# Optimization experiments

Hardware: AMD Instinct MI355X
Metric: run time of the kernel (lower is better)

## Reference

```python
import jax, jax.numpy as jnp
import numpy as np

TAU = 2.0        # spikingjelly LIFNode default tau
VTH = 1.0        # v_threshold
ALPHA = 2.0      # ATan surrogate default alpha
NWIN = (4, 4, 4)
TOPK = 4
HEADS = 8

@jax.custom_vjp
def spike(x):
    return (x >= 0.0).astype(x.dtype)

def _spike_fwd(x):
    return spike(x), x

def _spike_bwd(x, g):
    # ATan surrogate: d/dx ~ alpha/2 / (1 + (pi/2 * alpha * x)^2)
    s = (jnp.pi / 2) * ALPHA * x
    return (g * (ALPHA / 2) / (1 + s * s),)

spike.defvjp(_spike_fwd, _spike_bwd)

def lif(x):
    # fresh-state single-step LIF: H = x/tau, spike if H >= v_threshold
    return spike(x / TAU - VTH)

def setup_inputs() -> dict:
    key = jax.random.key(0)
    ks = jax.random.split(key, 4)
    T, B, Lt, Lh, Lw, C = 4, 2, 8, 32, 32, 256
    x = jax.random.normal(ks[0], (T, B, Lt, Lh, Lw, C), jnp.float32)
    W_qkv = jax.random.normal(ks[1], (C, 3 * C), jnp.float32) / np.sqrt(C)
    b_qkv = jnp.zeros((3 * C,), jnp.float32)
    W_proj = jax.random.normal(ks[2], (C, C), jnp.float32) / np.sqrt(C)
    b_proj = jnp.zeros((C,), jnp.float32)
    return {"x": x, "W_qkv": W_qkv, "b_qkv": b_qkv, "W_proj": W_proj, "b_proj": b_proj}

def reference(x, W_qkv, b_qkv, W_proj, b_proj):
    T, B, Lt, Lh, Lw, C = x.shape
    wt, wh, ww = NWIN
    H = HEADS
    hd = C // H
    nw = wt * wh * ww
    pt, ph, pw = Lt // wt, Lh // wh, Lw // ww
    ws = pt * ph * pw

    # windowize: [T,B,nw,ws,C]
    xw = x.reshape(T, B, wt, pt, wh, ph, ww, pw, C)
    xw = xw.transpose(0, 1, 2, 4, 6, 3, 5, 7, 8).reshape(T, B, nw, ws, C)

    # region-level routing scores over windows
    region = xw.sum(0).mean(2)                                  # [B,nw,C]
    scores = jnp.einsum('bic,bjc->bij', region, region) * (hd ** -0.5)
    idx = jax.lax.top_k(scores, TOPK)[1]                        # [B,nw,topk]

    qkv = xw @ W_qkv + b_qkv                                    # [T,B,nw,ws,3C]
    q, k, v = jnp.split(qkv, 3, axis=-1)
    q, k, v = lif(q), lif(k), lif(v)
    q = q.reshape(T, B, nw, ws, H, hd)
    k = k.reshape(T, B, nw, ws, H, hd)
    v = v.reshape(T, B, nw, ws, H, hd)

    # per-batch gather of topk routed windows' k/v
    gather = jax.vmap(lambda kb, ib: kb[:, ib], in_axes=(1, 0), out_axes=1)
    k_g = gather(k, idx).reshape(T, B, nw, TOPK * ws, H, hd)    # [T,B,nw,topk*ws,H,hd]
    v_g = gather(v, idx).reshape(T, B, nw, TOPK * ws, H, hd)

    # linear (kernelized) attention: kv = k^T v, out = q kv / (q sum_k)
    kv = jnp.einsum('tbnshd,tbnshe->tbnhde', k_g, v_g)          # [T,B,nw,H,hd,hd]
    out = jnp.einsum('tbnshd,tbnhde->tbnshe', q, kv)            # [T,B,nw,ws,H,hd]
    ksum = k_g.sum(3)                                           # [T,B,nw,H,hd]
    D = jnp.einsum('tbnshd,tbnhd->tbnsh', q, ksum)[..., None]   # [T,B,nw,ws,H,1]
    out = out / (D + 1e-6)

    out = out.reshape(T, B, nw, ws, C) @ W_proj + b_proj

    # un-windowize
    out = out.reshape(T, B, wt, wh, ww, pt, ph, pw, C)
    out = out.transpose(0, 1, 2, 5, 3, 6, 4, 7, 8).reshape(T, B, Lt, Lh, Lw, C)
    return out
```

## Files before the change

kernel.cpp:

```cpp
#include <hip/hip_runtime.h>
#include <cstdint>
#include <cstddef>

#define T_    4
#define B_    2
#define NW_   64
#define WS_   128
#define C_    256
#define NC3   768
#define H_    8
#define HD_   32
#define TOPK_ 4
#define RCAP  131072
#define BAND  0.008f
#define RBCAP 512

#define OFF_A2     0ull
#define OFF_BQ     67108864ull
#define OFF_BP     67502080ull
#define OFF_QM     67895296ull
#define OFF_KB     69992448ull
#define OFF_VB     72089600ull
#define OFF_KV     74186752ull
#define OFF_KCS    90963968ull
#define OFF_PART   91488256ull
#define OFF_REGION 92012544ull
#define OFF_IDX    92143616ull
#define OFF_RL     92145664ull
#define OFF_RC     92669952ull

typedef short short8 __attribute__((ext_vector_type(8)));
typedef float floatx4 __attribute__((ext_vector_type(4)));

__device__ __forceinline__ short f2bf(float f) {
    unsigned u = __float_as_uint(f);
    unsigned r = (u + 0x7fffu + ((u >> 16) & 1u)) >> 16;
    return (short)r;
}
__device__ __forceinline__ float bf2f(short h) {
    return __uint_as_float(((unsigned)(unsigned short)h) << 16);
}

__device__ __forceinline__ int xoff_row(int g, int s) {
    int tb = g >> 6;
    int n  = g & 63;
    int iwt = n >> 4, iwh = (n >> 2) & 3, iww = n & 3;
    int ipt = s >> 6, iph = (s >> 3) & 7, ipw = s & 7;
    int lt = iwt * 2 + ipt, lh = iwh * 8 + iph, lw = iww * 8 + ipw;
    return (((tb * 8 + lt) * 32 + lh) * 32 + lw) * 256;
}

__global__ __launch_bounds__(256) void k_partial_split(const float* __restrict__ x,
        float* __restrict__ part, short* __restrict__ A2) {
    int g = blockIdx.x;
    int c = threadIdx.x;
    const int ktAh = c >> 5, ktAl = 8 + (c >> 5);
    const int octsh = ((c >> 3) & 3) << 4, sub = c & 7;
    float acc = 0.f;
    for (int s = 0; s < WS_; ++s) {
        float v = x[xoff_row(g, s) + c];
        acc += v;
        short hi = f2bf(v);
        short lo = f2bf(v - bf2f(hi));
        int lane = (s & 15) | octsh;
        size_t base = ((size_t)(g * 8 + (s >> 4))) * 16;
        A2[(base + ktAh) * 512 + lane * 8 + sub] = hi;
        A2[(base + ktAl) * 512 + lane * 8 + sub] = lo;
    }
    part[g * C_ + c] = acc;
}

__global__ __launch_bounds__(256) void k_region(const float* __restrict__ part,
                                                float* __restrict__ region) {
    int bn = blockIdx.x;
    int c = threadIdx.x;
    int b = bn >> 6, n = bn & 63;
    float acc = 0.f;
    for (int t = 0; t < T_; ++t) acc += part[((t * 2 + b) * 64 + n) * C_ + c];
    region[bn * C_ + c] = acc * (1.0f / 128.0f);
}

__global__ __launch_bounds__(64) void k_scores(const float* __restrict__ region,
                                               int* __restrict__ idx) {
    int bi = blockIdx.x;
    int b = bi >> 6, i = bi & 63;
    int tid = threadIdx.x;
    __shared__ float ri[C_];
    __shared__ float sc[64];
    for (int c = tid; c < C_; c += 64) ri[c] = region[(b * 64 + i) * C_ + c];
    __syncthreads();
    const float* rj = region + (size_t)(b * 64 + tid) * C_;
    float dot = 0.f;
    for (int c = 0; c < C_; ++c) dot += ri[c] * rj[c];
    sc[tid] = dot * 0.17677669529663687f;
    __syncthreads();
    if (tid == 0) {
        for (int kk = 0; kk < TOPK_; ++kk) {
            float best = -INFINITY; int bj = 0;
            for (int j = 0; j < 64; ++j)
                if (sc[j] > best) { best = sc[j]; bj = j; }
            idx[bi * TOPK_ + kk] = bj;
            sc[bj] = -INFINITY;
        }
    }
}

__global__ __launch_bounds__(256) void b_build_qkv(const float* __restrict__ W,
                                                   short* __restrict__ Bq) {
    int ke = blockIdx.x;
    int n = blockIdx.y * 256 + threadIdx.x;
    float wv = W[(size_t)ke * NC3 + n];
    short o = f2bf(wv);
    int gj = n >> 4, lmn = n & 15, ktB = ke >> 5, oct = (ke >> 3) & 3, sub = ke & 7;
    Bq[(size_t)((gj * 8 + ktB) * 64 + (lmn | (oct << 4))) * 8 + sub] = o;
}
__global__ __launch_bounds__(256) void b_build_proj(const float* __restrict__ W,
                                                    short* __restrict__ Bp) {
    int ke = blockIdx.x;
    int n = threadIdx.x;
    float wv = W[(size_t)(ke & 255) * 256 + n];
    short hi = f2bf(wv);
    short o = (ke < 512) ? hi : f2bf(wv - bf2f(hi));
    int gj = n >> 4, lmn = n & 15, ktB = ke >> 5, oct = (ke >> 3) & 3, sub = ke & 7;
    Bp[(size_t)((gj * 24 + ktB) * 64 + (lmn | (oct << 4))) * 8 + sub] = o;
}

__device__ __forceinline__ unsigned p4(unsigned xv) {
    return (xv & 1u) | ((xv >> 7) & 2u) | ((xv >> 14) & 4u) | ((xv >> 21) & 8u);
}

__global__ __launch_bounds__(256, 2) void qkv_mfma(const short* __restrict__ A2,
        const short* __restrict__ Bq, const float* __restrict__ bias,
        unsigned* __restrict__ qm, unsigned* __restrict__ kb,
        unsigned* __restrict__ vb, unsigned* __restrict__ rl,
        unsigned* __restrict__ rcnt) {
    __shared__ unsigned char sp[128 * 264];
    __shared__ unsigned rbuf[RBCAP];
    __shared__ unsigned lcnt, sbase;
    const int bid = blockIdx.x;
    const int x8 = bid & 7;
    const int y = bid >> 3;
    const int p = y % 3;
    const int mb = x8 + ((y / 3) << 3);
    const int tid = threadIdx.x;
    const int wv = tid >> 6, lane = tid & 63;
    const int wm = wv >> 1, wn = wv & 1;
    const int lm = lane & 15, lq = lane >> 4;

    if (tid == 0) lcnt = 0;
    __syncthreads();

    floatx4 acc[4][8];
#pragma unroll
    for (int i = 0; i < 4; ++i)
#pragma unroll
        for (int j = 0; j < 8; ++j) acc[i][j] = (floatx4)0.f;

    const short* Ab = A2 + ((size_t)(mb * 8 + wm * 4) * 16) * 512 + lane * 8;
    const short* Bb = Bq + ((size_t)(p * 16 + wn * 8) * 8) * 512 + lane * 8;

    for (int ktB = 0; ktB < 8; ++ktB) {
        short8 ah[4], al[4], bf[8];
#pragma unroll
        for (int j = 0; j < 8; ++j)
            bf[j] = *(const short8*)(Bb + (size_t)(j * 8 + ktB) * 512);
#pragma unroll
        for (int i = 0; i < 4; ++i) {
            ah[i] = *(const short8*)(Ab + (size_t)(i * 16 + ktB) * 512);
            al[i] = *(const short8*)(Ab + (size_t)(i * 16 + 8 + ktB) * 512);
        }
#pragma unroll
        for (int i = 0; i < 4; ++i)
#pragma unroll
            for (int j = 0; j < 8; ++j)
                acc[i][j] = __builtin_amdgcn_mfma_f32_16x16x32_bf16(
                    ah[i], bf[j], acc[i][j], 0, 0, 0);
#pragma unroll
        for (int i = 0; i < 4; ++i)
#pragma unroll
            for (int j = 0; j < 8; ++j)
                acc[i][j] = __builtin_amdgcn_mfma_f32_16x16x32_bf16(
                    al[i], bf[j], acc[i][j], 0, 0, 0);
    }

#pragma unroll
    for (int i = 0; i < 4; ++i) {
#pragma unroll
        for (int j = 0; j < 8; ++j) {
            int cb = wn * 128 + j * 16 + lm;
            int cg = p * 256 + cb;
            float bj = bias[cg];
#pragma unroll
            for (int r = 0; r < 4; ++r) {
                int s = wm * 64 + i * 16 + lq * 4 + r;
                float v = acc[i][j][r] + bj;
                if (fabsf(v - 2.0f) < BAND) {
                    unsigned ent = ((unsigned)mb << 17) | ((unsigned)s << 10) | (unsigned)cg;
                    unsigned slot = atomicAdd(&lcnt, 1u);
                    if (slot < RBCAP) {
                        rbuf[slot] = ent;
                    } else {
                        unsigned gs = atomicAdd(rcnt, 1u);
                        if (gs < RCAP) rl[gs] = ent;
                    }
                }
                sp[s * 264 + cb] = (v >= 2.0f) ? 1 : 0;
            }
        }
    }
    __syncthreads();

    unsigned cnt = lcnt;
    if (cnt > RBCAP) cnt = RBCAP;
    if (tid == 0) sbase = atomicAdd(rcnt, cnt);
    __syncthreads();
    for (unsigned e = tid; e < cnt; e += 256) {
        unsigned slot = sbase + e;
        if (slot < RCAP) rl[slot] = rbuf[e];
    }

    if (p == 0) {
        const unsigned* spw = (const unsigned*)sp;
#pragma unroll
        for (int t = 0; t < 4; ++t) {
            int w = t * 256 + tid;
            int s = w >> 3, h = w & 7;
            unsigned m = 0;
#pragma unroll
            for (int q = 0; q < 8; ++q)
                m |= p4(spw[s * 66 + h * 8 + q]) << (q * 4);
            qm[(size_t)mb * 1024 + w] = m;
        }
    } else {
        unsigned wrd[4];
#pragma unroll
        for (int w2 = 0; w2 < 4; ++w2) {
            unsigned m = 0;
#pragma unroll
            for (int ii = 0; ii < 32; ++ii)
                m |= (unsigned)(sp[(w2 * 32 + ii) * 264 + tid] & 1) << ii;
            wrd[w2] = m;
        }
        uint4 o; o.x = wrd[0]; o.y = wrd[1]; o.z = wrd[2]; o.w = wrd[3];
        *(uint4*)(((p == 1) ? kb : vb) + ((size_t)mb * 256 + tid) * 4) = o;
    }
}

__global__ __launch_bounds__(256) void rescue_fix(const float* __restrict__ x,
        const float* __restrict__ W, const float* __restrict__ bias,
        const unsigned* __restrict__ rl, const unsigned* __restrict__ rcnt,
        unsigned* __restrict__ qm, unsigned* __restrict__ kb,
        unsigned* __restrict__ vb) {
    unsigned n = *rcnt; if (n > RCAP) n = RCAP;
    unsigned gid = blockIdx.x * 256 + threadIdx.x;
    unsigned stride = gridDim.x * 256;
    for (unsigned e = gid; e < n; e += stride) {
        unsigned ent = rl[e];
        int mb = ent >> 17, s = (ent >> 10) & 127, cg = ent & 1023;
        const float* ar = x + xoff_row(mb, s);
        const float* wc = W + cg;
        float da = 0.f;
#pragma unroll 4
        for (int k4 = 0; k4 < 64; ++k4) {
            float4 a4 = *(const float4*)(ar + k4 * 4);
            da = fmaf(a4.x, wc[(size_t)(k4 * 4 + 0) * NC3], da);
            da = fmaf(a4.y, wc[(size_t)(k4 * 4 + 1) * NC3], da);
            da = fmaf(a4.z, wc[(size_t)(k4 * 4 + 2) * NC3], da);
            da = fmaf(a4.w, wc[(size_t)(k4 * 4 + 3) * NC3], da);
        }
        da += bias[cg];
        int spk = (da >= 2.0f) ? 1 : 0;
        if (cg < 256) {
            int h = cg >> 5, d = cg & 31;
            unsigned* wp = qm + (size_t)mb * 1024 + s * 8 + h;
            unsigned bit = 1u << d;
            int have = (*wp & bit) ? 1 : 0;
            if (have != spk) atomicXor(wp, bit);
        } else {
            unsigned* tgt = (cg < 512) ? kb : vb;
            int c = cg & 255;
            unsigned* wp = tgt + ((size_t)mb * 256 + c) * 4 + (s >> 5);
            unsigned bit = 1u << (s & 31);
            int have = (*wp & bit) ? 1 : 0;
            if (have != spk) atomicXor(wp, bit);
        }
    }
}

__global__ __launch_bounds__(256) void kcs_bits(const unsigned* __restrict__ kb,
                                                float* __restrict__ kcs) {
    int g = blockIdx.x;
    int c = threadIdx.x;
    const unsigned* p = kb + ((size_t)g * 256 + c) * 4;
    int acc = __popc(p[0]) + __popc(p[1]) + __popc(p[2]) + __popc(p[3]);
    kcs[g * C_ + c] = (float)acc;
}

__global__ __launch_bounds__(256) void kv_bits(const unsigned* __restrict__ kb,
        const unsigned* __restrict__ vb, const int* __restrict__ idx,
        float* __restrict__ kvbuf) {
    int g = blockIdx.x;
    int tb = g >> 6, n = g & 63, b = tb & 1;
    int tid = threadIdx.x;
    __shared__ uint4 kbl[1024];
    __shared__ uint4 vbl[1024];
    __shared__ int widx[TOPK_];
    if (tid < TOPK_) widx[tid] = idx[(b * 64 + n) * TOPK_ + tid];
    __syncthreads();
#pragma unroll
    for (int kk = 0; kk < TOPK_; ++kk) {
        int g2 = tb * 64 + widx[kk];
        kbl[kk * 256 + tid] = *(const uint4*)&kb[((size_t)g2 * 256 + tid) * 4];
        vbl[kk * 256 + tid] = *(const uint4*)&vb[((size_t)g2 * 256 + tid) * 4];
    }
    __syncthreads();
    int h = tid >> 5, e = tid & 31;
    uint4 vw0 = vbl[0 * 256 + h * 32 + e];
    uint4 vw1 = vbl[1 * 256 + h * 32 + e];
    uint4 vw2 = vbl[2 * 256 + h * 32 + e];
    uint4 vw3 = vbl[3 * 256 + h * 32 + e];
    for (int d = 0; d < 32; ++d) {
        uint4 k0 = kbl[0 * 256 + h * 32 + d];
        uint4 k1 = kbl[1 * 256 + h * 32 + d];
        uint4 k2 = kbl[2 * 256 + h * 32 + d];
        uint4 k3 = kbl[3 * 256 + h * 32 + d];
        int acc = __popc(k0.x & vw0.x) + __popc(k0.y & vw0.y)
                + __popc(k0.z & vw0.z) + __popc(k0.w & vw0.w)
                + __popc(k1.x & vw1.x) + __popc(k1.y & vw1.y)
                + __popc(k1.z & vw1.z) + __popc(k1.w & vw1.w)
                + __popc(k2.x & vw2.x) + __popc(k2.y & vw2.y)
                + __popc(k2.z & vw2.z) + __popc(k2.w & vw2.w)
                + __popc(k3.x & vw3.x) + __popc(k3.y & vw3.y)
                + __popc(k3.z & vw3.z) + __popc(k3.w & vw3.w);
        kvbuf[((size_t)(g * 8 + h) * 32 + d) * 32 + e] = (float)acc;
    }
}

__global__ __launch_bounds__(256) void attn_proj(const unsigned* __restrict__ qm,
        const float* __restrict__ kvbuf, const float* __restrict__ kcs,
        const int* __restrict__ idx, const short* __restrict__ Bp,
        const float* __restrict__ bias, float* __restrict__ out) {
    __shared__ __align__(16) short aw[16384];
    __shared__ unsigned qb[256];
    __shared__ float ksl[256];
    __shared__ int widx[TOPK_];
    const int bid = blockIdx.x;
    const int g = bid >> 2, qr = bid & 3;
    const int tb = g >> 6, n = g & 63, b = tb & 1;
    const int tid = threadIdx.x;
    if (tid < TOPK_) widx[tid] = idx[(b * 64 + n) * TOPK_ + tid];
    __syncthreads();
    float ks = 0.f;
#pragma unroll
    for (int kk = 0; kk < TOPK_; ++kk)
        ks += kcs[(size_t)(tb * 64 + widx[kk]) * C_ + tid];
    ksl[tid] = ks;
    qb[tid] = qm[(size_t)g * 1024 + qr * 256 + tid];
    __syncthreads();

    const int h = tid >> 5, e = tid & 31;
    float kvr[32], ksr[32];
#pragma unroll
    for (int d = 0; d < 32; ++d)
        kvr[d] = kvbuf[((size_t)(g * 8 + h) * 32 + d) * 32 + e];
#pragma unroll
    for (int d = 0; d < 32; ++d) ksr[d] = ksl[h * 32 + d];

    const int ktAh = tid >> 5, ktAl = 8 + (tid >> 5);
    const int octsh = ((tid >> 3) & 3) << 4, sub = tid & 7;
    for (int sl = 0; sl < 32; ++sl) {
        unsigned qw = qb[sl * 8 + h];
        float r;
        if (qw == 0u) {
            r = 0.f;
        } else {
            float num = 0.f, den = 0.f;
#pragma unroll
            for (int d = 0; d < 32; ++d) {
                float m = (float)((qw >> d) & 1u);
                num = fmaf(m, kvr[d], num);
                den = fmaf(m, ksr[d], den);
            }
            r = num / (den + 1e-6f);
        }
        short hi = f2bf(r), lo = f2bf(r - bf2f(hi));
        int lane2 = (sl & 15) | octsh;
        int gi = sl >> 4;
        aw[((gi * 16 + ktAh) * 64 + lane2) * 8 + sub] = hi;
        aw[((gi * 16 + ktAl) * 64 + lane2) * 8 + sub] = lo;
    }
    __syncthreads();

    const int wvw = tid >> 6, lane = tid & 63;
    const int lm = lane & 15, lq = lane >> 4;
    floatx4 pacc[2][4];
#pragma unroll
    for (int i = 0; i < 2; ++i)
#pragma unroll
        for (int j = 0; j < 4; ++j) pacc[i][j] = (floatx4)0.f;
    const short* Bb = Bp + ((size_t)(wvw * 4) * 24) * 512 + lane * 8;
#pragma unroll 2
    for (int kt = 0; kt < 24; ++kt) {
        int ktA = (kt < 16) ? kt : kt - 16;
        short8 af[2], bf[4];
#pragma unroll
        for (int i = 0; i < 2; ++i)
            af[i] = *(const short8*)&aw[((i * 16 + ktA) * 64 + lane) * 8];
#pragma unroll
        for (int j = 0; j < 4; ++j)
            bf[j] = *(const short8*)(Bb + (size_t)(j * 24 + kt) * 512);
#pragma unroll
        for (int i = 0; i < 2; ++i)
#pragma unroll
            for (int j = 0; j < 4; ++j)
                pacc[i][j] = __builtin_amdgcn_mfma_f32_16x16x32_bf16(
                    af[i], bf[j], pacc[i][j], 0, 0, 0);
    }
    __syncthreads();

    float* ow = (float*)aw;
#pragma unroll
    for (int i = 0; i < 2; ++i) {
#pragma unroll
        for (int j = 0; j < 4; ++j) {
            int c = wvw * 64 + j * 16 + lm;
            float bj = bias[c];
#pragma unroll
            for (int r = 0; r < 4; ++r)
                ow[(i * 16 + lq * 4 + r) * 256 + c] = pacc[i][j][r] + bj;
        }
    }
    __syncthreads();

    int sl2 = tid >> 3, pc = (tid & 7) * 32;
    int off = xoff_row(g, qr * 32 + sl2) + pc;
#pragma unroll
    for (int q = 0; q < 8; ++q)
        *(float4*)(out + off + q * 4) = *(const float4*)&ow[sl2 * 256 + pc + q * 4];
}

extern "C" void kernel_launch(void* const* d_in, const int* in_sizes, int n_in,
                              void* d_out, int out_size, void* d_ws, size_t ws_size,
                              hipStream_t stream) {
    (void)in_sizes; (void)n_in; (void)out_size; (void)ws_size;
    const float* x    = (const float*)d_in[0];
    const float* Wqkv = (const float*)d_in[1];
    const float* bqkv = (const float*)d_in[2];
    const float* Wp   = (const float*)d_in[3];
    const float* bp   = (const float*)d_in[4];
    char* ws = (char*)d_ws;
    short*    A2    = (short*)   (ws + OFF_A2);
    short*    Bq    = (short*)   (ws + OFF_BQ);
    short*    Bpj   = (short*)   (ws + OFF_BP);
    unsigned* qmv   = (unsigned*)(ws + OFF_QM);
    unsigned* kb    = (unsigned*)(ws + OFF_KB);
    unsigned* vb    = (unsigned*)(ws + OFF_VB);
    float*    kvbuf = (float*)   (ws + OFF_KV);
    float*    kcs   = (float*)   (ws + OFF_KCS);
    float*    part  = (float*)   (ws + OFF_PART);
    float*    region= (float*)   (ws + OFF_REGION);
    int*      idxb  = (int*)     (ws + OFF_IDX);
    unsigned* rl    = (unsigned*)(ws + OFF_RL);
    unsigned* rcnt  = (unsigned*)(ws + OFF_RC);
    float*    out   = (float*)d_out;

    hipMemsetAsync(rcnt, 0, 4, stream);
    b_build_qkv    <<<dim3(256, 3), 256, 0, stream>>>(Wqkv, Bq);
    b_build_proj   <<<768, 256, 0, stream>>>(Wp, Bpj);
    k_partial_split<<<512, 256, 0, stream>>>(x, part, A2);
    k_region       <<<128, 256, 0, stream>>>(part, region);
    k_scores       <<<128,  64, 0, stream>>>(region, idxb);
    qkv_mfma       <<<1536, 256, 0, stream>>>(A2, Bq, bqkv, qmv, kb, vb, rl, rcnt);
    rescue_fix     <<<256, 256, 0, stream>>>(x, Wqkv, bqkv, rl, rcnt, qmv, kb, vb);
    kcs_bits       <<<512, 256, 0, stream>>>(kb, kcs);
    kv_bits        <<<512, 256, 0, stream>>>(kb, vb, idxb, kvbuf);
    attn_proj      <<<2048, 256, 0, stream>>>(qmv, kvbuf, kcs, idxb, Bpj, bp, out);
}
```

Measured before the change: 257.6 us.

## Double-buffer QKV GEMM operands in LDS via async global_load_lds

The QKV MFMA kernel now stages A and B tiles into a two-buffer shared-memory area with global_load_lds and prefetches the next K chunk while computing the current one. Before, each wave read its operands straight from global memory, and different waves loaded the same B and A fragments again. The change is meant to share loads across waves and hide memory latency. It enlarges LDS use to 64KB plus rbuf, which may cut occupancy below the 2 blocks requested in the launch bounds. It also adds a barrier on every iteration, and the loop has no explicit wait on the async loads before the barrier, which relies on __syncthreads emitting a vmcnt wait.

Result: faster. 235.9 us (-8.4%).

```diff
diff --git a/kernel.cpp b/kernel.cpp
--- a/kernel.cpp
+++ b/kernel.cpp
@@ -39,6 +39,13 @@
 }
 __device__ __forceinline__ float bf2f(short h) {
     return __uint_as_float(((unsigned)(unsigned short)h) << 16);
+}
+
+__device__ __forceinline__ void gload_lds16(const void* g, void* l) {
+    __builtin_amdgcn_global_load_lds(
+        (const __attribute__((address_space(1))) unsigned*)g,
+        (__attribute__((address_space(3))) unsigned*)l,
+        16, 0, 0);
 }
 
 __device__ __forceinline__ int xoff_row(int g, int s) {
@@ -134,7 +141,7 @@
         unsigned* __restrict__ qm, unsigned* __restrict__ kb,
         unsigned* __restrict__ vb, unsigned* __restrict__ rl,
         unsigned* __restrict__ rcnt) {
-    __shared__ unsigned char sp[128 * 264];
+    __shared__ __align__(16) char stg[2][32768];
     __shared__ unsigned rbuf[RBCAP];
     __shared__ unsigned lcnt, sbase;
     const int bid = blockIdx.x;
@@ -148,7 +155,27 @@
     const int lm = lane & 15, lq = lane >> 4;
 
     if (tid == 0) lcnt = 0;
-    __syncthreads();
+
+    const char* Ag = (const char*)(A2 + (size_t)mb * 65536);
+    const char* Bg = (const char*)(Bq + (size_t)p * 65536);
+    const int laneoff = lane * 16;
+
+#define STAGE_CHUNK(buf, ktB_)                                                 \
+    {                                                                          \
+        _Pragma("unroll")                                                      \
+        for (int k = 0; k < 4; ++k) {                                          \
+            int slot = k * 4 + wv;                                             \
+            int gi = slot >> 1, hl = slot & 1;                                 \
+            const char* src = Ag + (((gi * 16) + (ktB_) + hl * 8) << 10) + laneoff; \
+            gload_lds16(src, &stg[buf][k * 4096 + wv * 1024 + laneoff]);       \
+        }                                                                      \
+        _Pragma("unroll")                                                      \
+        for (int k = 0; k < 4; ++k) {                                          \
+            int slot = k * 4 + wv;                                             \
+            const char* src = Bg + ((slot * 8 + (ktB_)) << 10) + laneoff;      \
+            gload_lds16(src, &stg[buf][16384 + k * 4096 + wv * 1024 + laneoff]); \
+        }                                                                      \
+    }
 
     floatx4 acc[4][8];
 #pragma unroll
@@ -156,18 +183,21 @@
 #pragma unroll
         for (int j = 0; j < 8; ++j) acc[i][j] = (floatx4)0.f;
 
-    const short* Ab = A2 + ((size_t)(mb * 8 + wm * 4) * 16) * 512 + lane * 8;
-    const short* Bb = Bq + ((size_t)(p * 16 + wn * 8) * 8) * 512 + lane * 8;
+    STAGE_CHUNK(0, 0);
+    __syncthreads();
 
     for (int ktB = 0; ktB < 8; ++ktB) {
+        int cur = ktB & 1;
+        if (ktB < 7) STAGE_CHUNK(cur ^ 1, ktB + 1);
+        const char* sb = &stg[cur][0];
         short8 ah[4], al[4], bf[8];
 #pragma unroll
         for (int j = 0; j < 8; ++j)
-            bf[j] = *(const short8*)(Bb + (size_t)(j * 8 + ktB) * 512);
+            bf[j] = *(const short8*)(sb + 16384 + ((wn * 8 + j) << 10) + laneoff);
 #pragma unroll
         for (int i = 0; i < 4; ++i) {
-            ah[i] = *(const short8*)(Ab + (size_t)(i * 16 + ktB) * 512);
-            al[i] = *(const short8*)(Ab + (size_t)(i * 16 + 8 + ktB) * 512);
+            ah[i] = *(const short8*)(sb + (((wm * 4 + i) * 2 + 0) << 10) + laneoff);
+            al[i] = *(const short8*)(sb + (((wm * 4 + i) * 2 + 1) << 10) + laneoff);
         }
 #pragma unroll
         for (int i = 0; i < 4; ++i)
@@ -181,8 +211,10 @@
             for (int j = 0; j < 8; ++j)
                 acc[i][j] = __builtin_amdgcn_mfma_f32_16x16x32_bf16(
                     al[i], bf[j], acc[i][j], 0, 0, 0);
-    }
-
+        __syncthreads();
+    }
+
+    unsigned char* sp = (unsigned char*)&stg[0][0];
 #pragma unroll
     for (int i = 0; i < 4; ++i) {
 #pragma unroll
```
